# Optimization experiments

Hardware: AMD Instinct MI355X
Metric: run time of the kernel (lower is better)

## Reference

```python
import jax, jax.numpy as jnp
import numpy as np

D_LATENTS = 256
B, N = 8, 4096
EPS = 1e-5  # BatchNorm eps (torch default)


def _w(k, shape):
    return jax.random.normal(k, shape, jnp.float32) * 0.05


def setup_inputs() -> dict:
    key = jax.random.key(0)
    ks = jax.random.split(key, 20)
    d4, d2, d = D_LATENTS // 4, D_LATENTS // 2, D_LATENTS
    def bn(k):
        k1, k2 = jax.random.split(k)
        g = 1.0 + 0.1 * jax.random.normal(k1, (0,), jnp.float32)  # placeholder
        return g
    inp = {
        "x": jax.random.normal(ks[0], (B, 3, N), jnp.float32),
        "conv1_w": _w(ks[1], (d4, 3)),
        "bn1_g": 1.0 + 0.1 * jax.random.normal(ks[2], (d4,), jnp.float32),
        "bn1_b": 0.1 * jax.random.normal(ks[3], (d4,), jnp.float32),
        "conv2_w": _w(ks[4], (d4, d4)),
        "bn2_g": 1.0 + 0.1 * jax.random.normal(ks[5], (d4,), jnp.float32),
        "bn2_b": 0.1 * jax.random.normal(ks[6], (d4,), jnp.float32),
        "le0_w1": _w(ks[7], (d2, d2)),
        "le0_g1": 1.0 + 0.1 * jax.random.normal(ks[8], (d2,), jnp.float32),
        "le0_b1": 0.1 * jax.random.normal(ks[9], (d2,), jnp.float32),
        "le0_w2": _w(ks[10], (d2, d2)),
        "le0_g2": 1.0 + 0.1 * jax.random.normal(ks[11], (d2,), jnp.float32),
        "le0_b2": 0.1 * jax.random.normal(ks[12], (d2,), jnp.float32),
        "le1_w1": _w(ks[13], (d, d)),
        "le1_g1": 1.0 + 0.1 * jax.random.normal(ks[14], (d,), jnp.float32),
        "le1_b1": 0.1 * jax.random.normal(ks[15], (d,), jnp.float32),
        "le1_w2": _w(ks[16], (d, d)),
        "le1_g2": 1.0 + 0.1 * jax.random.normal(ks[17], (d,), jnp.float32),
        "le1_b2": 0.1 * jax.random.normal(ks[18], (d,), jnp.float32),
    }
    return inp


def _bn_relu(y, g, b, axes, ch_axis):
    # BatchNorm (training-mode batch stats, biased var like torch) + ReLU
    m = jnp.mean(y, axes, keepdims=True)
    v = jnp.var(y, axes, keepdims=True)
    shp = [1] * y.ndim
    shp[ch_axis] = -1
    return jax.nn.relu((y - m) * jax.lax.rsqrt(v + EPS) * g.reshape(shp) + b.reshape(shp))


def _square_distance(src, dst):
    # src [B,S,3], dst [B,N,3] -> [B,S,N]
    return (jnp.sum(src * src, -1, keepdims=True)
            - 2.0 * jnp.einsum('bsc,bnc->bsn', src, dst)
            + jnp.sum(dst * dst, -1)[:, None, :])


def _fps(xyz, npoint):
    # farthest point sampling, deterministic start at index 0
    Bb, Nn, _ = xyz.shape
    def step(carry, _):
        dist_min, farthest = carry
        centroid = jnp.take_along_axis(xyz, farthest[:, None, None], axis=1)  # [B,1,3]
        d = jnp.sum((xyz - centroid) ** 2, -1)  # [B,N]
        dist_min = jnp.minimum(dist_min, d)
        nxt = jnp.argmax(dist_min, -1).astype(jnp.int32)
        return (dist_min, nxt), farthest
    init = (jnp.full((Bb, Nn), 1e10, xyz.dtype), jnp.zeros((Bb,), jnp.int32))
    _, idxs = jax.lax.scan(step, init, None, length=npoint)
    return jnp.transpose(idxs)  # [B, npoint]


def _sample_and_group(npoint, nsample, xyz, points):
    # PCT-style: FPS centers, kNN neighbors (radius unused), concat(rel, center)
    Bb = xyz.shape[0]
    fps_idx = _fps(xyz, npoint)                       # [B,S]
    bidx = jnp.arange(Bb)[:, None]
    new_xyz = xyz[bidx, fps_idx]                      # [B,S,3]
    new_pts = points[bidx, fps_idx]                   # [B,S,D]
    d2 = _square_distance(new_xyz, xyz)               # [B,S,N]
    _, knn_idx = jax.lax.top_k(-d2, nsample)          # [B,S,ns]
    grouped = points[jnp.arange(Bb)[:, None, None], knn_idx]  # [B,S,ns,D]
    center = new_pts[:, :, None, :]
    feat = jnp.concatenate([grouped - center,
                            jnp.broadcast_to(center, grouped.shape)], axis=-1)
    return new_xyz, feat  # [B,S,3], [B,S,ns,2D]


def _local_encoder(x4, w1, g1, b1, w2, g2, b2):
    # x4: [b,n,s,d] -> conv1x1/bn/relu x2 over channel dim, max over s -> [b,out,n]
    y = jnp.einsum('bnsd,od->bnos', x4, w1)
    y = _bn_relu(y, g1, b1, (0, 1, 3), 2)
    y = jnp.einsum('bnis,oi->bnos', y, w2)
    y = _bn_relu(y, g2, b2, (0, 1, 3), 2)
    y = jnp.max(y, axis=3)                # [b,n,out]
    return jnp.transpose(y, (0, 2, 1))    # [b,out,n]


def reference(x, conv1_w, bn1_g, bn1_b, conv2_w, bn2_g, bn2_b,
              le0_w1, le0_g1, le0_b1, le0_w2, le0_g2, le0_b2,
              le1_w1, le1_g1, le1_b1, le1_w2, le1_g2, le1_b2):
    xyz = jnp.transpose(x, (0, 2, 1))                 # [B,N,3]
    y = jnp.einsum('bcn,oc->bon', x, conv1_w)
    y = _bn_relu(y, bn1_g, bn1_b, (0, 2), 1)
    y = jnp.einsum('bcn,oc->bon', y, conv2_w)
    y = _bn_relu(y, bn2_g, bn2_b, (0, 2), 1)
    pts = jnp.transpose(y, (0, 2, 1))                 # [B,N,d4]
    new_xyz, feat = _sample_and_group(512, 32, xyz, pts)       # [B,512,32,d2]
    f0 = _local_encoder(feat, le0_w1, le0_g1, le0_b1, le0_w2, le0_g2, le0_b2)  # [B,d2,512]
    pts1 = jnp.transpose(f0, (0, 2, 1))
    _, feat2 = _sample_and_group(256, 32, new_xyz, pts1)       # [B,256,32,d]
    f1 = _local_encoder(feat2, le1_w1, le1_g1, le1_b1, le1_w2, le1_g2, le1_b2)  # [B,d,256]
    return f1
```

## Files before the change

### kernel.cpp

```cpp
#include <hip/hip_runtime.h>

constexpr int B_  = 8;
constexpr int N_  = 4096;
constexpr int NP1 = 512;
constexpr int NP2 = 256;
constexpr float EPS_ = 1e-5f;

typedef __attribute__((ext_vector_type(8))) short bhalf8;
typedef __attribute__((ext_vector_type(4))) float f32x4;

__device__ inline short f2bf(float f) {
  union { float fv; unsigned u; } v; v.fv = f;
  unsigned r = v.u + 0x7FFFu + ((v.u >> 16) & 1u);
  return (short)(r >> 16);
}

template<int CTRL>
__device__ inline void dpp_amax(unsigned &khi, unsigned &klo) {
  unsigned ohi = (unsigned)__builtin_amdgcn_mov_dpp((int)khi, CTRL, 0xF, 0xF, false);
  unsigned olo = (unsigned)__builtin_amdgcn_mov_dpp((int)klo, CTRL, 0xF, 0xF, false);
  if (ohi > khi || (ohi == khi && olo > klo)) { khi = ohi; klo = olo; }
}
__device__ inline void swz16_amax(unsigned &khi, unsigned &klo) {
  unsigned ohi = (unsigned)__builtin_amdgcn_ds_swizzle((int)khi, 0x401F);
  unsigned olo = (unsigned)__builtin_amdgcn_ds_swizzle((int)klo, 0x401F);
  if (ohi > khi || (ohi == khi && olo > klo)) { khi = ohi; klo = olo; }
}
__device__ inline void x32_amax(unsigned &khi, unsigned &klo) {
  unsigned ohi = (unsigned)__shfl_xor((int)khi, 32);
  unsigned olo = (unsigned)__shfl_xor((int)klo, 32);
  if (ohi > khi || (ohi == khi && olo > klo)) { khi = ohi; klo = olo; }
}

constexpr int S_BN1 = 0;
constexpr int S_BN2 = 128;
constexpr int S_L0A = 256;
constexpr int S_L0B = 512;
constexpr int S_L1A = 768;
constexpr int S_L1B = 1280;
constexpr int S_TOTAL = 1792;

constexpr size_t OFF_T1   = 0;
constexpr size_t OFF_YBUF = OFF_T1   + 2097152;
constexpr size_t OFF_PTS1 = OFF_YBUF + 16777216;
constexpr size_t OFF_NXYZ = OFF_PTS1 + 524288;
constexpr size_t OFF_WT2C = OFF_NXYZ + 12288;
constexpr size_t OFF_BW0A = OFF_WT2C + 4096;
constexpr size_t OFF_BW0B = OFF_BW0A + 8192;
constexpr size_t OFF_BW1A = OFF_BW0B + 8192;
constexpr size_t OFF_BW1B = OFF_BW1A + 32768;
constexpr size_t OFF_STAT = OFF_BW1B + 32768;
constexpr size_t OFF_INT  = OFF_STAT + 1792;

__global__ void prep_kernel(const float* __restrict__ conv2w,
                            const float* __restrict__ w0a, const float* __restrict__ w0b,
                            const float* __restrict__ w1a, const float* __restrict__ w1b,
                            float* __restrict__ wt2c,
                            short* __restrict__ b0a, short* __restrict__ b0b,
                            short* __restrict__ b1a, short* __restrict__ b1b) {
  int idx = blockIdx.x * 256 + threadIdx.x;
  if (idx < 4096) { int d = idx >> 6, o = idx & 63; wt2c[idx] = conv2w[o*64 + d]; return; }
  idx -= 4096;
  const float* w; short* dst; int D;
  if      (idx <  2048) { w = w0a; dst = b0a; D = 128; }
  else if (idx <  4096) { w = w0b; dst = b0b; D = 128; idx -= 2048; }
  else if (idx < 12288) { w = w1a; dst = b1a; D = 256; idx -= 4096; }
  else if (idx < 20480) { w = w1b; dst = b1b; D = 256; idx -= 12288; }
  else return;
  int kblk = idx / D, o = idx % D;
  const float* src = w + (size_t)o*D + kblk*8;
  bhalf8 pk;
#pragma unroll
  for (int j = 0; j < 8; ++j) pk[j] = f2bf(src[j]);
  *(bhalf8*)&dst[(size_t)idx*8] = pk;
}

__global__ __launch_bounds__(256) void conv1_kernel(
    const float* __restrict__ x, const float* __restrict__ w,
    float* __restrict__ t1, float* __restrict__ stats) {
  __shared__ float xs[3][64];
  __shared__ float redS[4][64], redQ[4][64];
  int blk = blockIdx.x;
  int b = blk >> 6, n0 = (blk & 63) << 6;
  int t = threadIdx.x;
  if (t < 192) { int c = t >> 6, nl = t & 63; xs[c][nl] = x[((size_t)b*3 + c)*N_ + n0 + nl]; }
  __syncthreads();
  int o = t & 63, ng = t >> 6;
  float w0 = w[o*3+0], w1 = w[o*3+1], w2 = w[o*3+2];
  float ls = 0.f, lq = 0.f;
#pragma unroll
  for (int k = 0; k < 16; ++k) {
    int nl = ng*16 + k;
    float y = xs[0][nl]*w0 + xs[1][nl]*w1 + xs[2][nl]*w2;
    t1[((size_t)b*N_ + n0 + nl)*64 + o] = y;
    ls += y; lq += y*y;
  }
  redS[ng][o] = ls; redQ[ng][o] = lq;
  __syncthreads();
  if (t < 64) {
    float s = redS[0][t]+redS[1][t]+redS[2][t]+redS[3][t];
    float q = redQ[0][t]+redQ[1][t]+redQ[2][t]+redQ[3][t];
    atomicAdd(&stats[S_BN1 + t], s);
    atomicAdd(&stats[S_BN1 + 64 + t], q);
  }
}

__global__ __launch_bounds__(256) void conv2_kernel(
    const float* __restrict__ t1, const float* __restrict__ g1, const float* __restrict__ b1,
    const float* __restrict__ wt2c, float* __restrict__ t2, float* __restrict__ stats) {
  constexpr int P = 68;
  __shared__ float at[64*P];
  __shared__ float sc[64], sh[64];
  __shared__ float redS[4][64], redQ[4][64];
  int blk = blockIdx.x;
  int b = blk >> 6, n0 = (blk & 63) << 6;
  int t = threadIdx.x;
  if (t < 64) {
    float m = stats[S_BN1 + t] * (1.f/32768.f);
    float v = stats[S_BN1 + 64 + t] * (1.f/32768.f) - m*m;
    float s = g1[t] * rsqrtf(v + EPS_);
    sc[t] = s; sh[t] = b1[t] - m*s;
  }
  __syncthreads();
  for (int e = t; e < 4096; e += 256) {
    int nl = e >> 6, c = e & 63;
    float v = t1[((size_t)b*N_ + n0 + nl)*64 + c];
    at[c*P + nl] = fmaxf(v*sc[c] + sh[c], 0.f);
  }
  __syncthreads();
  int o = t & 63, ng = t >> 6;
  float acc[16];
#pragma unroll
  for (int k = 0; k < 16; ++k) acc[k] = 0.f;
  for (int i = 0; i < 64; ++i) {
    float wv = wt2c[i*64 + o];
    const float* ar = &at[i*P + ng*16];
#pragma unroll
    for (int k = 0; k < 16; k += 4) {
      float4 a4 = *(const float4*)(ar + k);
      acc[k+0] += a4.x*wv; acc[k+1] += a4.y*wv;
      acc[k+2] += a4.z*wv; acc[k+3] += a4.w*wv;
    }
  }
  float ls = 0.f, lq = 0.f;
#pragma unroll
  for (int k = 0; k < 16; ++k) {
    float y = acc[k];
    t2[((size_t)b*N_ + n0 + ng*16 + k)*64 + o] = y;
    ls += y; lq += y*y;
  }
  redS[ng][o] = ls; redQ[ng][o] = lq;
  __syncthreads();
  if (t < 64) {
    float s = redS[0][t]+redS[1][t]+redS[2][t]+redS[3][t];
    float q = redQ[0][t]+redQ[1][t]+redQ[2][t]+redQ[3][t];
    atomicAdd(&stats[S_BN2 + t], s);
    atomicAdd(&stats[S_BN2 + 64 + t], q);
  }
}

__global__ __launch_bounds__(256) void bn2fin_kernel(
    const float* __restrict__ t2, const float* __restrict__ g2, const float* __restrict__ b2,
    const float* __restrict__ stats, float* __restrict__ pts) {
  int idx = blockIdx.x*256 + threadIdx.x;
  int o = idx & 63;
  float m = stats[S_BN2 + o] * (1.f/32768.f);
  float v = stats[S_BN2 + 64 + o] * (1.f/32768.f) - m*m;
  float s = g2[o] * rsqrtf(v + EPS_);
  pts[idx] = fmaxf(t2[idx]*s + (b2[o] - m*s), 0.f);
}

template<int NPTS, int NSEL1, int NSEL2, int NT>
__global__ __launch_bounds__(NT) void fps_fused_kernel(
    const float* __restrict__ x,
    int* __restrict__ sel1, float* __restrict__ nxyz, int* __restrict__ sel2) {
  constexpr int K  = NPTS / NT;
  constexpr int NS = NT / 32;
  __shared__ float lx[NPTS], ly[NPTS], lz[NPTS];
  __shared__ float sx[NSEL1], sy[NSEL1], sz[NSEL1];
  __shared__ unsigned long long wk[2][NS];
  __shared__ int seli1[NSEL1];
  __shared__ int seli2[NSEL2];
  int b = blockIdx.x, t = threadIdx.x;
  int lane = t & 63, wid = t >> 6;
  const float* cb = x + (size_t)b * 3 * NPTS;
  for (int i = t; i < NPTS; i += NT) {
    lx[i] = cb[i]; ly[i] = cb[NPTS + i]; lz[i] = cb[2*NPTS + i];
  }
  __syncthreads();
  float px[K], py[K], pz[K], dm[K];
#pragma unroll
  for (int k = 0; k < K; ++k) {
    int p = t + k*NT;
    px[k] = lx[p]; py[k] = ly[p]; pz[k] = lz[p];
    dm[k] = 1e10f;
  }
  float cx = lx[0], cy = ly[0], cz = lz[0];
  if (t == 0) { seli1[0] = 0; sx[0] = cx; sy[0] = cy; sz[0] = cz; }
  for (int it = 1; it < NSEL1; ++it) {
    float bv = -1.f; int bi = 0;
#pragma unroll
    for (int k = 0; k < K; ++k) {
      float dx = px[k]-cx, dy = py[k]-cy, dz = pz[k]-cz;
      float d = dx*dx + dy*dy + dz*dz;
      float nd = fminf(dm[k], d);
      dm[k] = nd;
      if (nd > bv) { bv = nd; bi = t + k*NT; }
    }
    unsigned khi = __float_as_uint(bv), klo = ~(unsigned)bi;
    dpp_amax<0xB1>(khi, klo);
    dpp_amax<0x4E>(khi, klo);
    dpp_amax<0x141>(khi, klo);
    dpp_amax<0x140>(khi, klo);
    swz16_amax(khi, klo);
    int p = it & 1;
    if ((lane & 31) == 0)
      wk[p][wid*2 + (lane >> 5)] = ((unsigned long long)khi << 32) | klo;
    __syncthreads();
    unsigned long long best = wk[p][0];
#pragma unroll
    for (int i2 = 1; i2 < NS; ++i2) { unsigned long long v2 = wk[p][i2]; if (v2 > best) best = v2; }
    int Bi = (int)(~(unsigned)best);
    cx = lx[Bi]; cy = ly[Bi]; cz = lz[Bi];
    if (t == 0) { seli1[it] = Bi; sx[it] = cx; sy[it] = cy; sz[it] = cz; }
  }
  __syncthreads();
  if (t < 64) {
    constexpr int K2 = NSEL1 / 64;
    float qx[K2], qy[K2], qz[K2], dm2[K2];
#pragma unroll
    for (int k = 0; k < K2; ++k) {
      int p = t + k*64;
      qx[k] = sx[p]; qy[k] = sy[p]; qz[k] = sz[p];
      dm2[k] = 1e10f;
    }
    cx = sx[0]; cy = sy[0]; cz = sz[0];
    if (t == 0) seli2[0] = 0;
    for (int it = 1; it < NSEL2; ++it) {
      float bv = -1.f; int bi = 0;
#pragma unroll
      for (int k = 0; k < K2; ++k) {
        float dx = qx[k]-cx, dy = qy[k]-cy, dz = qz[k]-cz;
        float d = dx*dx + dy*dy + dz*dz;
        float nd = fminf(dm2[k], d);
        dm2[k] = nd;
        if (nd > bv) { bv = nd; bi = t + k*64; }
      }
      unsigned khi = __float_as_uint(bv), klo = ~(unsigned)bi;
      dpp_amax<0xB1>(khi, klo);
      dpp_amax<0x4E>(khi, klo);
      dpp_amax<0x141>(khi, klo);
      dpp_amax<0x140>(khi, klo);
      swz16_amax(khi, klo);
      x32_amax(khi, klo);
      int Bi = (int)~klo;
      cx = sx[Bi]; cy = sy[Bi]; cz = sz[Bi];
      if (t == 0) seli2[it] = Bi;
    }
  } else {
    for (int i = t - 64; i < NSEL1; i += NT - 64) {
      sel1[(size_t)b*NSEL1 + i] = seli1[i];
      float* q = nxyz + ((size_t)b*NSEL1 + i)*3;
      q[0] = sx[i]; q[1] = sy[i]; q[2] = sz[i];
    }
  }
  __syncthreads();
  for (int i = t; i < NSEL2; i += NT) sel2[(size_t)b*NSEL2 + i] = seli2[i];
}

template<int NDST, int NQ, int NT, bool XLAY>
__global__ __launch_bounds__(NT) void knn_kernel(
    const float* __restrict__ dst, const float* __restrict__ nxyz,
    const int* __restrict__ qmap, int* __restrict__ knn_out) {
  constexpr int K = NDST / NT;
  constexpr int NW = NT / 64;
  __shared__ float d2s[NDST];
  __shared__ float wvs[NW]; __shared__ int wis[NW];
  int blk = blockIdx.x, t = threadIdx.x;
  int b = blk / NQ, q = blk % NQ;
  int qrow = b*NP1 + (qmap ? qmap[b*NQ + q] : q);
  float qx = nxyz[qrow*3+0], qy = nxyz[qrow*3+1], qz = nxyz[qrow*3+2];
  float q2 = (qx*qx + qy*qy) + qz*qz;
  const float* db = dst + (size_t)b * (XLAY ? 3*NDST : NDST*3);
#pragma unroll
  for (int k = 0; k < K; ++k) {
    int j = t + k*NT;
    float xx, yy, zz;
    if (XLAY) { xx = db[j]; yy = db[NDST + j]; zz = db[2*NDST + j]; }
    else      { xx = db[j*3]; yy = db[j*3+1]; zz = db[j*3+2]; }
    float dot = (qx*xx + qy*yy) + qz*zz;
    float p2  = (xx*xx + yy*yy) + zz*zz;
    d2s[j] = (q2 - 2.f*dot) + p2;
  }
  __syncthreads();
  int lane = t & 63, wid = t >> 6;
  int* ko = knn_out + ((size_t)b*NQ + q)*32;
  for (int r = 0; r < 32; ++r) {
    float bv = 3e38f; int bi = NDST;
#pragma unroll
    for (int k = 0; k < K; ++k) {
      int j = t + k*NT;
      float v = d2s[j];
      if (v < bv || (v == bv && j < bi)) { bv = v; bi = j; }
    }
#pragma unroll
    for (int off = 1; off < 64; off <<= 1) {
      float ov = __shfl_xor(bv, off);
      int   oi = __shfl_xor(bi, off);
      if (ov < bv || (ov == bv && oi < bi)) { bv = ov; bi = oi; }
    }
    if (lane == 0) { wvs[wid] = bv; wis[wid] = bi; }
    __syncthreads();
    if (t == 0) {
      float Bv = wvs[0]; int Bi = wis[0];
      for (int w = 1; w < NW; ++w)
        if (wvs[w] < Bv || (wvs[w] == Bv && wis[w] < Bi)) { Bv = wvs[w]; Bi = wis[w]; }
      ko[r] = Bi;
      d2s[Bi] = 3e38f;
    }
    __syncthreads();
  }
}

template<int D, int PW, int NP, int SRCN, int SOFF>
__global__ __launch_bounds__(256) void gemm1_kernel(
    const float* __restrict__ pts, const int* __restrict__ knn,
    const int* __restrict__ cent, const short* __restrict__ bw,
    float* __restrict__ ybuf, float* __restrict__ stats) {
  constexpr int KB = D/8;
  __shared__ __align__(16) short As[64*D];
  __shared__ float cen_s[2*PW];
  __shared__ int kid_s[64];
  __shared__ float sstat[2*D];
  int t = threadIdx.x, blk = blockIdx.x;
  int g0 = blk*2;
  if (t < 64) {
    int grp = t >> 5, s = t & 31;
    kid_s[t] = knn[((size_t)(g0+grp))*32 + s];
  }
  for (int i = t; i < 2*PW; i += 256) {
    int grp = i / PW, d = i % PW;
    int g = g0 + grp; int b = g / NP; int ci = cent[g];
    cen_s[i] = pts[((size_t)b*SRCN + ci)*PW + d];
  }
  for (int i = t; i < 2*D; i += 256) sstat[i] = 0.f;
  __syncthreads();
  for (int task = t; task < 64*KB; task += 256) {
    int row = task / KB, c = task % KB;
    int grp = row >> 5;
    int g = g0 + grp; int b = g / NP;
    int d = c*8;
    float v0,v1,v2,v3,v4,v5,v6,v7;
    if (d < PW) {
      const float* src = pts + ((size_t)b*SRCN + kid_s[row])*PW + d;
      float4 x0 = *(const float4*)src, x1 = *(const float4*)(src+4);
      const float* cc = &cen_s[grp*PW + d];
      v0=x0.x-cc[0]; v1=x0.y-cc[1]; v2=x0.z-cc[2]; v3=x0.w-cc[3];
      v4=x1.x-cc[4]; v5=x1.y-cc[5]; v6=x1.z-cc[6]; v7=x1.w-cc[7];
    } else {
      const float* cc = &cen_s[grp*PW + d - PW];
      v0=cc[0]; v1=cc[1]; v2=cc[2]; v3=cc[3]; v4=cc[4]; v5=cc[5]; v6=cc[6]; v7=cc[7];
    }
    bhalf8 pk;
    pk[0]=f2bf(v0); pk[1]=f2bf(v1); pk[2]=f2bf(v2); pk[3]=f2bf(v3);
    pk[4]=f2bf(v4); pk[5]=f2bf(v5); pk[6]=f2bf(v6); pk[7]=f2bf(v7);
    int a16 = row*KB + (c ^ (row & 7));
    *(bhalf8*)&As[a16*8] = pk;
  }
  __syncthreads();
  int w = t >> 6, l = t & 63, lr = l & 15, lg = l >> 4;
  f32x4 acc[D/16];
#pragma unroll
  for (int ct = 0; ct < D/16; ++ct) acc[ct] = (f32x4){0.f,0.f,0.f,0.f};
  int r = w*16 + lr;
#pragma unroll
  for (int kg = 0; kg < D/32; ++kg) {
    int c = (kg*4 + lg) ^ (r & 7);
    bhalf8 af = *(const bhalf8*)&As[(r*KB + c)*8];
#pragma unroll
    for (int ct = 0; ct < D/16; ++ct) {
      bhalf8 bf = *(const bhalf8*)&bw[((size_t)(kg*4 + lg)*D + ct*16 + lr)*8];
      acc[ct] = __builtin_amdgcn_mfma_f32_16x16x32_bf16(af, bf, acc[ct], 0, 0, 0);
    }
  }
  size_t rb = (size_t)blk*64 + w*16 + lg*4;
#pragma unroll
  for (int ct = 0; ct < D/16; ++ct) {
    int col = ct*16 + lr;
    f32x4 a = acc[ct];
    float* yp = ybuf + rb*D + col;
    yp[0] = a[0]; yp[(size_t)D] = a[1]; yp[(size_t)2*D] = a[2]; yp[(size_t)3*D] = a[3];
    float s = a[0]+a[1]+a[2]+a[3];
    float q = a[0]*a[0]+a[1]*a[1]+a[2]*a[2]+a[3]*a[3];
    s += __shfl_xor(s, 16); q += __shfl_xor(q, 16);
    s += __shfl_xor(s, 32); q += __shfl_xor(q, 32);
    if (lg == 0) { atomicAdd(&sstat[col], s); atomicAdd(&sstat[D+col], q); }
  }
  __syncthreads();
  for (int i = t; i < 2*D; i += 256) atomicAdd(&stats[SOFF+i], sstat[i]);
}

template<int D, int SIN, int SOUT, int CNT>
__global__ __launch_bounds__(256) void gemm2_kernel(
    const float* __restrict__ g1, const float* __restrict__ b1,
    const short* __restrict__ bw, float* __restrict__ ybuf, float* __restrict__ stats) {
  __shared__ __align__(16) float scsh[2*D];
  __shared__ float sstat[2*D];
  int t = threadIdx.x, blk = blockIdx.x;
  for (int i = t; i < D; i += 256) {
    float m = stats[SIN + i] * (1.f/(float)CNT);
    float v = stats[SIN + D + i] * (1.f/(float)CNT) - m*m;
    float s = g1[i] * rsqrtf(v + EPS_);
    scsh[i] = s; scsh[D+i] = b1[i] - m*s;
  }
  for (int i = t; i < 2*D; i += 256) sstat[i] = 0.f;
  __syncthreads();
  int w = t >> 6, l = t & 63, lr = l & 15, lg = l >> 4;
  size_t row = (size_t)blk*64 + w*16 + lr;
  const float* yrow = ybuf + row*D;
  f32x4 acc[D/16];
#pragma unroll
  for (int ct = 0; ct < D/16; ++ct) acc[ct] = (f32x4){0.f,0.f,0.f,0.f};
#pragma unroll
  for (int kg = 0; kg < D/32; ++kg) {
    int k = kg*32 + lg*8;
    float4 y0 = *(const float4*)(yrow + k);
    float4 y1 = *(const float4*)(yrow + k + 4);
    bhalf8 af;
    af[0] = f2bf(fmaxf(y0.x*scsh[k+0] + scsh[D+k+0], 0.f));
    af[1] = f2bf(fmaxf(y0.y*scsh[k+1] + scsh[D+k+1], 0.f));
    af[2] = f2bf(fmaxf(y0.z*scsh[k+2] + scsh[D+k+2], 0.f));
    af[3] = f2bf(fmaxf(y0.w*scsh[k+3] + scsh[D+k+3], 0.f));
    af[4] = f2bf(fmaxf(y1.x*scsh[k+4] + scsh[D+k+4], 0.f));
    af[5] = f2bf(fmaxf(y1.y*scsh[k+5] + scsh[D+k+5], 0.f));
    af[6] = f2bf(fmaxf(y1.z*scsh[k+6] + scsh[D+k+6], 0.f));
    af[7] = f2bf(fmaxf(y1.w*scsh[k+7] + scsh[D+k+7], 0.f));
#pragma unroll
    for (int ct = 0; ct < D/16; ++ct) {
      bhalf8 bf = *(const bhalf8*)&bw[((size_t)(kg*4 + lg)*D + ct*16 + lr)*8];
      acc[ct] = __builtin_amdgcn_mfma_f32_16x16x32_bf16(af, bf, acc[ct], 0, 0, 0);
    }
  }
  size_t rb = (size_t)blk*64 + w*16 + lg*4;
#pragma unroll
  for (int ct = 0; ct < D/16; ++ct) {
    int col = ct*16 + lr;
    f32x4 a = acc[ct];
    float* yp = ybuf + rb*D + col;
    yp[0] = a[0]; yp[(size_t)D] = a[1]; yp[(size_t)2*D] = a[2]; yp[(size_t)3*D] = a[3];
    float s = a[0]+a[1]+a[2]+a[3];
    float q = a[0]*a[0]+a[1]*a[1]+a[2]*a[2]+a[3]*a[3];
    s += __shfl_xor(s, 16); q += __shfl_xor(q, 16);
    s += __shfl_xor(s, 32); q += __shfl_xor(q, 32);
    if (lg == 0) { atomicAdd(&sstat[col], s); atomicAdd(&sstat[D+col], q); }
  }
  __syncthreads();
  for (int i = t; i < 2*D; i += 256) atomicAdd(&stats[SOUT+i], sstat[i]);
}

template<int D, int NP, int SOFF, int CNT, bool TR>
__global__ void le3_kernel(const float* __restrict__ g2, const float* __restrict__ b2,
                           const float* __restrict__ ybuf, const float* __restrict__ stats,
                           float* __restrict__ out) {
  int blk = blockIdx.x, o = threadIdx.x;
  int b = blk / NP, n = blk % NP;
  float m = stats[SOFF + o] * (1.f/(float)CNT);
  float v = stats[SOFF + D + o] * (1.f/(float)CNT) - m*m;
  float s = g2[o] * rsqrtf(v + EPS_);
  float sh = b2[o] - m*s;
  const float* yb = ybuf + ((size_t)(b*NP + n)*32)*D + o;
  float mx = 0.f;
#pragma unroll
  for (int k = 0; k < 32; ++k) mx = fmaxf(mx, yb[(size_t)k*D]*s + sh);
  if (TR) out[((size_t)b*D + o)*NP + n] = mx;
  else    out[((size_t)b*NP + n)*D + o] = mx;
}

extern "C" void kernel_launch(void* const* d_in, const int* in_sizes, int n_in,
                              void* d_out, int out_size, void* d_ws, size_t ws_size,
                              hipStream_t stream) {
  (void)in_sizes; (void)n_in; (void)out_size; (void)ws_size;
  const float* x       = (const float*)d_in[0];
  const float* conv1_w = (const float*)d_in[1];
  const float* bn1_g   = (const float*)d_in[2];
  const float* bn1_b   = (const float*)d_in[3];
  const float* conv2_w = (const float*)d_in[4];
  const float* bn2_g   = (const float*)d_in[5];
  const float* bn2_b   = (const float*)d_in[6];
  const float* le0_w1  = (const float*)d_in[7];
  const float* le0_g1  = (const float*)d_in[8];
  const float* le0_b1  = (const float*)d_in[9];
  const float* le0_w2  = (const float*)d_in[10];
  const float* le0_g2  = (const float*)d_in[11];
  const float* le0_b2  = (const float*)d_in[12];
  const float* le1_w1  = (const float*)d_in[13];
  const float* le1_g1  = (const float*)d_in[14];
  const float* le1_b1  = (const float*)d_in[15];
  const float* le1_w2  = (const float*)d_in[16];
  const float* le1_g2  = (const float*)d_in[17];
  const float* le1_b2  = (const float*)d_in[18];

  float* ws   = (float*)d_ws;
  float* t1   = ws + OFF_T1;
  float* ybuf = ws + OFF_YBUF;
  float* t2   = ybuf;
  float* pts1 = ws + OFF_PTS1;
  float* nxyz = ws + OFF_NXYZ;
  float* wt2c = ws + OFF_WT2C;
  short* bw0a = (short*)(ws + OFF_BW0A);
  short* bw0b = (short*)(ws + OFF_BW0B);
  short* bw1a = (short*)(ws + OFF_BW1A);
  short* bw1b = (short*)(ws + OFF_BW1B);
  float* stats = ws + OFF_STAT;
  int* fps1 = (int*)(ws + OFF_INT);
  int* fps2 = fps1 + 4096;
  int* knn1 = fps2 + 2048;
  int* knn2 = knn1 + 131072;

  hipMemsetAsync(stats, 0, S_TOTAL*sizeof(float), stream);
  prep_kernel<<<96, 256, 0, stream>>>(conv2_w, le0_w1, le0_w2, le1_w1, le1_w2,
                                      wt2c, bw0a, bw0b, bw1a, bw1b);
  conv1_kernel<<<512, 256, 0, stream>>>(x, conv1_w, t1, stats);
  conv2_kernel<<<512, 256, 0, stream>>>(t1, bn1_g, bn1_b, wt2c, t2, stats);
  bn2fin_kernel<<<8192, 256, 0, stream>>>(t2, bn2_g, bn2_b, stats, t1);

  fps_fused_kernel<4096, 512, 256, 256><<<8, 256, 0, stream>>>(x, fps1, nxyz, fps2);
  knn_kernel<4096, 512, 256, true ><<<4096, 256, 0, stream>>>(x, nxyz, nullptr, knn1);
  knn_kernel< 512, 256, 256, false><<<2048, 256, 0, stream>>>(nxyz, nxyz, fps2, knn2);

  gemm1_kernel<128,  64, 512, 4096, S_L0A><<<2048, 256, 0, stream>>>(t1, knn1, fps1, bw0a, ybuf, stats);
  gemm2_kernel<128, S_L0A, S_L0B, 131072><<<2048, 256, 0, stream>>>(le0_g1, le0_b1, bw0b, ybuf, stats);
  le3_kernel<128, 512, S_L0B, 131072, false><<<4096, 128, 0, stream>>>(le0_g2, le0_b2, ybuf, stats, pts1);

  gemm1_kernel<256, 128, 256,  512, S_L1A><<<1024, 256, 0, stream>>>(pts1, knn2, fps2, bw1a, ybuf, stats);
  gemm2_kernel<256, S_L1A, S_L1B, 65536><<<1024, 256, 0, stream>>>(le1_g1, le1_b1, bw1b, ybuf, stats);
  le3_kernel<256, 256, S_L1B, 65536, true><<<2048, 256, 0, stream>>>(le1_g2, le1_b2, ybuf, stats, (float*)d_out);
}
```

Baseline: 1.130 ms.

## Keep kNN distances in registers and replace second-GEMM output with per-group max/min

The kNN selection now keeps distances in registers, reduces argmin with DPP/swizzle packed 64-bit keys, and uses one barrier per round with a double-buffered shared slot instead of two barriers and a serial thread-0 step. The second GEMM no longer writes its full pre-BN activation to global memory. It records per-group column max and min, and the final BN+ReLU+max kernel picks max or min depending on the sign of the BN scale, using monotonicity. This removes a large write and re-read of the activation buffer, at the cost of extra shared memory and a reduction step in the GEMM epilogue.

Measured after the change: 1.020 ms. 9.7% less time.

```diff
diff --git a/kernel.cpp b/kernel.cpp
--- a/kernel.cpp
+++ b/kernel.cpp
@@ -30,6 +30,10 @@
   unsigned ohi = (unsigned)__shfl_xor((int)khi, 32);
   unsigned olo = (unsigned)__shfl_xor((int)klo, 32);
   if (ohi > khi || (ohi == khi && olo > klo)) { khi = ohi; klo = olo; }
+}
+__device__ inline unsigned ford(float f) {
+  unsigned u = __float_as_uint(f);
+  return u ^ (((unsigned)((int)u >> 31)) | 0x80000000u);
 }
 
 constexpr int S_BN1 = 0;
@@ -272,16 +276,17 @@
 __global__ __launch_bounds__(NT) void knn_kernel(
     const float* __restrict__ dst, const float* __restrict__ nxyz,
     const int* __restrict__ qmap, int* __restrict__ knn_out) {
-  constexpr int K = NDST / NT;
-  constexpr int NW = NT / 64;
-  __shared__ float d2s[NDST];
-  __shared__ float wvs[NW]; __shared__ int wis[NW];
+  constexpr int K  = NDST / NT;
+  constexpr int NS = NT / 32;
+  __shared__ unsigned long long wk[2][NS];
+  __shared__ int kos[32];
   int blk = blockIdx.x, t = threadIdx.x;
   int b = blk / NQ, q = blk % NQ;
   int qrow = b*NP1 + (qmap ? qmap[b*NQ + q] : q);
   float qx = nxyz[qrow*3+0], qy = nxyz[qrow*3+1], qz = nxyz[qrow*3+2];
   float q2 = (qx*qx + qy*qy) + qz*qz;
   const float* db = dst + (size_t)b * (XLAY ? 3*NDST : NDST*3);
+  float d2r[K];
 #pragma unroll
   for (int k = 0; k < K; ++k) {
     int j = t + k*NT;
@@ -290,36 +295,36 @@
     else      { xx = db[j*3]; yy = db[j*3+1]; zz = db[j*3+2]; }
     float dot = (qx*xx + qy*yy) + qz*zz;
     float p2  = (xx*xx + yy*yy) + zz*zz;
-    d2s[j] = (q2 - 2.f*dot) + p2;
-  }
-  __syncthreads();
-  int lane = t & 63, wid = t >> 6;
-  int* ko = knn_out + ((size_t)b*NQ + q)*32;
+    d2r[k] = (q2 - 2.f*dot) + p2;
+  }
   for (int r = 0; r < 32; ++r) {
-    float bv = 3e38f; int bi = NDST;
+    float bv = 3e38f; int bi = t;
 #pragma unroll
     for (int k = 0; k < K; ++k) {
-      int j = t + k*NT;
-      float v = d2s[j];
-      if (v < bv || (v == bv && j < bi)) { bv = v; bi = j; }
-    }
-#pragma unroll
-    for (int off = 1; off < 64; off <<= 1) {
-      float ov = __shfl_xor(bv, off);
-      int   oi = __shfl_xor(bi, off);
-      if (ov < bv || (ov == bv && oi < bi)) { bv = ov; bi = oi; }
-    }
-    if (lane == 0) { wvs[wid] = bv; wis[wid] = bi; }
+      float v = d2r[k];
+      if (v < bv) { bv = v; bi = t + k*NT; }
+    }
+    unsigned khi = ~ford(bv), klo = ~(unsigned)bi;
+    dpp_amax<0xB1>(khi, klo);
+    dpp_amax<0x4E>(khi, klo);
+    dpp_amax<0x141>(khi, klo);
+    dpp_amax<0x140>(khi, klo);
+    swz16_amax(khi, klo);
+    int p = r & 1;
+    if ((t & 31) == 0)
+      wk[p][t >> 5] = ((unsigned long long)khi << 32) | klo;
     __syncthreads();
-    if (t == 0) {
-      float Bv = wvs[0]; int Bi = wis[0];
-      for (int w = 1; w < NW; ++w)
-        if (wvs[w] < Bv || (wvs[w] == Bv && wis[w] < Bi)) { Bv = wvs[w]; Bi = wis[w]; }
-      ko[r] = Bi;
-      d2s[Bi] = 3e38f;
-    }
-    __syncthreads();
-  }
+    unsigned long long best = wk[p][0];
+#pragma unroll
+    for (int i2 = 1; i2 < NS; ++i2) { unsigned long long v2 = wk[p][i2]; if (v2 > best) best = v2; }
+    int Bi = (int)(~(unsigned)best);
+    if (t == 0) kos[r] = Bi;
+#pragma unroll
+    for (int k = 0; k < K; ++k)
+      if (t + k*NT == Bi) d2r[k] = 3e38f;
+  }
+  __syncthreads();
+  if (t < 32) knn_out[((size_t)b*NQ + q)*32 + t] = kos[t];
 }
 
 template<int D, int PW, int NP, int SRCN, int SOFF>
@@ -403,9 +408,11 @@
 template<int D, int SIN, int SOUT, int CNT>
 __global__ __launch_bounds__(256) void gemm2_kernel(
     const float* __restrict__ g1, const float* __restrict__ b1,
-    const short* __restrict__ bw, float* __restrict__ ybuf, float* __restrict__ stats) {
+    const short* __restrict__ bw, const float* __restrict__ ybuf,
+    float* __restrict__ mm, float* __restrict__ stats) {
   __shared__ __align__(16) float scsh[2*D];
   __shared__ float sstat[2*D];
+  __shared__ float wmax[4][D], wmin[4][D];
   int t = threadIdx.x, blk = blockIdx.x;
   for (int i = t; i < D; i += 256) {
     float m = stats[SIN + i] * (1.f/(float)CNT);
@@ -441,13 +448,15 @@
       acc[ct] = __builtin_amdgcn_mfma_f32_16x16x32_bf16(af, bf, acc[ct], 0, 0, 0);
     }
   }
-  size_t rb = (size_t)blk*64 + w*16 + lg*4;
 #pragma unroll
   for (int ct = 0; ct < D/16; ++ct) {
     int col = ct*16 + lr;
     f32x4 a = acc[ct];
-    float* yp = ybuf + rb*D + col;
-    yp[0] = a[0]; yp[(size_t)D] = a[1]; yp[(size_t)2*D] = a[2]; yp[(size_t)3*D] = a[3];
+    float mx = fmaxf(fmaxf(a[0], a[1]), fmaxf(a[2], a[3]));
+    float mn = fminf(fminf(a[0], a[1]), fminf(a[2], a[3]));
+    mx = fmaxf(mx, __shfl_xor(mx, 16)); mn = fminf(mn, __shfl_xor(mn, 16));
+    mx = fmaxf(mx, __shfl_xor(mx, 32)); mn = fminf(mn, __shfl_xor(mn, 32));
+    if (lg == 0) { wmax[w][col] = mx; wmin[w][col] = mn; }
     float s = a[0]+a[1]+a[2]+a[3];
     float q = a[0]*a[0]+a[1]*a[1]+a[2]*a[2]+a[3]*a[3];
     s += __shfl_xor(s, 16); q += __shfl_xor(q, 16);
@@ -455,25 +464,32 @@
     if (lg == 0) { atomicAdd(&sstat[col], s); atomicAdd(&sstat[D+col], q); }
   }
   __syncthreads();
-  for (int i = t; i < 2*D; i += 256) atomicAdd(&stats[SOUT+i], sstat[i]);
+  for (int i = t; i < 2*D; i += 256) {
+    int g = i / D, col = i - g*D;
+    float mx = fmaxf(wmax[2*g][col], wmax[2*g+1][col]);
+    float mn = fminf(wmin[2*g][col], wmin[2*g+1][col]);
+    float* mp = mm + ((size_t)blk*2 + g)*2*D;
+    mp[col] = mx; mp[D + col] = mn;
+    atomicAdd(&stats[SOUT+i], sstat[i]);
+  }
 }
 
 template<int D, int NP, int SOFF, int CNT, bool TR>
-__global__ void le3_kernel(const float* __restrict__ g2, const float* __restrict__ b2,
-                           const float* __restrict__ ybuf, const float* __restrict__ stats,
-                           float* __restrict__ out) {
-  int blk = blockIdx.x, o = threadIdx.x;
-  int b = blk / NP, n = blk % NP;
+__global__ __launch_bounds__(256) void le3_kernel(
+    const float* __restrict__ g2, const float* __restrict__ b2,
+    const float* __restrict__ mm, const float* __restrict__ stats,
+    float* __restrict__ out) {
+  int idx = blockIdx.x*256 + threadIdx.x;
+  int g = idx / D, o = idx - g*D;
   float m = stats[SOFF + o] * (1.f/(float)CNT);
   float v = stats[SOFF + D + o] * (1.f/(float)CNT) - m*m;
   float s = g2[o] * rsqrtf(v + EPS_);
   float sh = b2[o] - m*s;
-  const float* yb = ybuf + ((size_t)(b*NP + n)*32)*D + o;
-  float mx = 0.f;
-#pragma unroll
-  for (int k = 0; k < 32; ++k) mx = fmaxf(mx, yb[(size_t)k*D]*s + sh);
-  if (TR) out[((size_t)b*D + o)*NP + n] = mx;
-  else    out[((size_t)b*NP + n)*D + o] = mx;
+  const float* mp = mm + (size_t)g*2*D;
+  float pick = (s >= 0.f) ? mp[o] : mp[D + o];
+  float r = fmaxf(pick*s + sh, 0.f);
+  if (TR) { int b = g / NP, n = g - b*NP; out[((size_t)b*D + o)*NP + n] = r; }
+  else    out[(size_t)g*D + o] = r;
 }
 
 extern "C" void kernel_launch(void* const* d_in, const int* in_sizes, int n_in,
@@ -504,6 +520,7 @@
   float* t1   = ws + OFF_T1;
   float* ybuf = ws + OFF_YBUF;
   float* t2   = ybuf;
+  float* mm   = t1;
   float* pts1 = ws + OFF_PTS1;
   float* nxyz = ws + OFF_NXYZ;
   float* wt2c = ws + OFF_WT2C;
@@ -529,10 +546,10 @@
   knn_kernel< 512, 256, 256, false><<<2048, 256, 0, stream>>>(nxyz, nxyz, fps2, knn2);
 
   gemm1_kernel<128,  64, 512, 4096, S_L0A><<<2048, 256, 0, stream>>>(t1, knn1, fps1, bw0a, ybuf, stats);
-  gemm2_kernel<128, S_L0A, S_L0B, 131072><<<2048, 256, 0, stream>>>(le0_g1, le0_b1, bw0b, ybuf, stats);
-  le3_kernel<128, 512, S_L0B, 131072, false><<<4096, 128, 0, stream>>>(le0_g2, le0_b2, ybuf, stats, pts1);
+  gemm2_kernel<128, S_L0A, S_L0B, 131072><<<2048, 256, 0, stream>>>(le0_g1, le0_b1, bw0b, ybuf, mm, stats);
+  le3_kernel<128, 512, S_L0B, 131072, false><<<2048, 256, 0, stream>>>(le0_g2, le0_b2, mm, stats, pts1);
 
   gemm1_kernel<256, 128, 256,  512, S_L1A><<<1024, 256, 0, stream>>>(pts1, knn2, fps2, bw1a, ybuf, stats);
-  gemm2_kernel<256, S_L1A, S_L1B, 65536><<<1024, 256, 0, stream>>>(le1_g1, le1_b1, bw1b, ybuf, stats);
-  le3_kernel<256, 256, S_L1B, 65536, true><<<2048, 256, 0, stream>>>(le1_g2, le1_b2, ybuf, stats, (float*)d_out);
-}
+  gemm2_kernel<256, S_L1A, S_L1B, 65536><<<1024, 256, 0, stream>>>(le1_g1, le1_b1, bw1b, ybuf, mm, stats);
+  le3_kernel<256, 256, S_L1B, 65536, true><<<2048, 256, 0, stream>>>(le1_g2, le1_b2, mm, stats, (float*)d_out);
+}
```
